# Kernel optimization log

Hardware: AMD Instinct MI355X
Metric: run time of the kernel (lower is better)

Reference implementation:

```python
import jax, jax.numpy as jnp
import numpy as np

H = 50  # hidden_size
IN = 1  # input_size

def _lstm_layer(x_tbi, w_ih, w_hh, b):
    # x_tbi: [T, B, in]; w_ih: [4H, in]; w_hh: [4H, H]; b: [4H] (b_ih + b_hh combined)
    T, B, _ = x_tbi.shape
    def step(carry, x_t):
        h, c = carry
        z = x_t @ w_ih.T + h @ w_hh.T + b  # [B, 4H]
        i, f, g, o = jnp.split(z, 4, axis=-1)
        i = jax.nn.sigmoid(i); f = jax.nn.sigmoid(f)
        g = jnp.tanh(g); o = jax.nn.sigmoid(o)
        c = f * c + i * g
        h = o * jnp.tanh(c)
        return (h, c), h
    h0 = jnp.zeros((B, H), x_tbi.dtype)
    c0 = jnp.zeros((B, H), x_tbi.dtype)
    _, hs = jax.lax.scan(step, (h0, c0), x_tbi)
    return hs  # [T, B, H]

def setup_inputs() -> dict:
    key = jax.random.key(0)
    ks = jax.random.split(key, 12)
    def u(k, shape, fan):
        s = 1.0 / np.sqrt(fan)
        return jax.random.uniform(k, shape, jnp.float32, -s, s)
    B, T = 2048, 512
    x = jax.random.normal(ks[0], (B, T, IN), jnp.float32)
    return {
        'x': x,
        'w_ih1': u(ks[1], (4 * H, IN), H), 'w_hh1': u(ks[2], (4 * H, H), H), 'b1': u(ks[3], (4 * H,), H),
        'w_ih2': u(ks[4], (4 * H, H), H), 'w_hh2': u(ks[5], (4 * H, H), H), 'b2': u(ks[6], (4 * H,), H),
        'w_ih3': u(ks[7], (4 * H, H), H), 'w_hh3': u(ks[8], (4 * H, H), H), 'b3': u(ks[9], (4 * H,), H),
        'w_fc': u(ks[10], (1, H), H), 'b_fc': u(ks[11], (1,), H),
    }

def reference(x, w_ih1, w_hh1, b1, w_ih2, w_hh2, b2, w_ih3, w_hh3, b3, w_fc, b_fc):
    # dropout layers act as identity in eval mode
    out = jnp.transpose(x, (1, 0, 2))  # [T, B, in]
    out = _lstm_layer(out, w_ih1, w_hh1, b1)
    out = _lstm_layer(out, w_ih2, w_hh2, b2)
    out = _lstm_layer(out, w_ih3, w_hh3, b3)
    last = out[-1]  # [B, H]
    return last @ w_fc.T + b_fc  # [B, 1]
```

## Files before the change

kernel.cpp:

```cpp
#include <hip/hip_runtime.h>
#include <math.h>

namespace {

constexpr int Hn = 50;
constexpr int Bn = 2048;
constexpr int Tn = 512;
constexpr int SW = 72;

constexpr float KS1f = -1.44269504088896340736f;
constexpr float KS2f = -2.88539008177792681472f;

typedef short short8 __attribute__((ext_vector_type(8)));
typedef float f32x4 __attribute__((ext_vector_type(4)));

__device__ __forceinline__ unsigned bcu(float f) { return __builtin_bit_cast(unsigned, f); }
__device__ __forceinline__ float bcf(unsigned u) { return __builtin_bit_cast(float, u); }
__device__ __forceinline__ float rcpa(float x) { return __builtin_amdgcn_rcpf(x); }

__device__ __forceinline__ float fexp2(float x) {
#if defined(__has_builtin)
#if __has_builtin(__builtin_amdgcn_exp2f)
  return __builtin_amdgcn_exp2f(x);
#else
  return exp2f(x);
#endif
#else
  return exp2f(x);
#endif
}

__device__ __forceinline__ void wsplit(short* ph, short* pl, float v) {
  const unsigned u = bcu(v);
  *ph = (short)(u >> 16);
  *pl = (short)(bcu(v - bcf(u & 0xFFFF0000u)) >> 16);
}

#define MF(a, b, c) __builtin_amdgcn_mfma_f32_16x16x32_bf16(a, b, c, 0, 0, 0)


#define LW(FI)                                                               \
  short8 FH##FI = {0, 0, 0, 0, 0, 0, 0, 0};                                  \
  short8 FL##FI = {0, 0, 0, 0, 0, 0, 0, 0};                                  \
  {                                                                          \
    const int tile_ =                                                        \
        ((FI) >= 16) ? ((L == 0 || wl != 0) ? 13 : 12)                       \
        : ((FI) >= 8) ? ((L == 0) ? 13 : (wl + 8))                           \
        : (L == 0)    ? (wl + 4 * ((FI) >> 1))                               \
                      : (wl + 4 * ((FI) >> 2));                              \
    const int chunk_ = ((FI) >= 8) ? ((FI)&3)                                \
                       : (L == 0)  ? ((FI)&1)                                \
                                   : ((FI)&3);                               \
    const int cb_ = 4 * tile_ + (nl >> 2);                                   \
    if (tile_ < 13 && cb_ < Hn) {                                            \
      const int row_ = (nl & 3) * Hn + cb_;                                  \
      const float sc_ = ((nl & 3) == 2) ? KS2f : KS1f;                       \
      _Pragma("unroll") for (int jj = 0; jj < 8; ++jj) {                     \
        const int k_ = 32 * chunk_ + quad * 8 + jj;                          \
        float wv = 0.f;                                                      \
        if (L == 0) {                                                        \
          if (k_ == 0) wv = wihL[row_];                                      \
          else if (k_ <= Hn) wv = whhL[row_ * Hn + k_ - 1];                  \
        } else if (L == 1) {                                                 \
          if (k_ >= 1 && k_ <= Hn) wv = wihL[row_ * Hn + k_ - 1];            \
          else if (k_ >= 64 && k_ < 64 + Hn) wv = whhL[row_ * Hn + k_ - 64]; \
        } else {                                                             \
          if (k_ < Hn) wv = wihL[row_ * Hn + k_];                            \
          else if (k_ >= 64 && k_ < 64 + Hn) wv = whhL[row_ * Hn + k_ - 64]; \
        }                                                                    \
        wv *= sc_;                                                           \
        const unsigned uu = bcu(wv);                                         \
        FH##FI[jj] = (short)(uu >> 16);                                      \
        FL##FI[jj] = (short)(bcu(wv - bcf(uu & 0xFFFF0000u)) >> 16);         \
      }                                                                      \
    }                                                                        \
  }

#define BINIT(J)                                                             \
  const int tile##J = wl + 4 * (J);                                          \
  const int tv##J = tile##J < 13;                                            \
  const int cell##J = 4 * tile##J + quad;                                    \
  float cs##J = 0.f, hl##J = 0.f;

#define STB(J)                                                               \
  if (tv##J) {                                                               \
    float b0_ = 0.f, b1_ = 0.f, b2_ = 0.f, b3_ = 0.f;                        \
    if (cell##J < Hn) {                                                      \
      b0_ = biasL[cell##J] * KS1f;                                           \
      b1_ = biasL[Hn + cell##J] * KS1f;                                      \
      b2_ = biasL[2 * Hn + cell##J] * KS2f;                                  \
      b3_ = biasL[3 * Hn + cell##J] * KS1f;                                  \
    }                                                                        \
    s_bv[w][J][quad][0] = b0_;                                               \
    s_bv[w][J][quad][1] = b1_;                                               \
    s_bv[w][J][quad][2] = b2_;                                               \
    s_bv[w][J][quad][3] = b3_;                                               \
  }

#define MTM(J, FI)                                                           \
  if (tv##J) {                                                               \
    ac##J = MF(FH##FI, uh_, ac##J);                                          \
    ac##J = MF(FL##FI, uh_, ac##J);                                          \
    ac##J = MF(FH##FI, ul_, ac##J);                                          \
  }

#define MTMS2(CI)                                                            \
  {                                                                          \
    const short8 fh_ = s_f4j2[wz2][wl][CI][0][lane];                         \
    const short8 fl_ = s_f4j2[wz2][wl][CI][1][lane];                         \
    ac2 = MF(fh_, uh_, ac2);                                                 \
    ac2 = MF(fl_, uh_, ac2);                                                 \
    ac2 = MF(fh_, ul_, ac2);                                                 \
  }

#define MTMS3(CI)                                                            \
  if (tv3) {                                                                 \
    const short8 fh_ = s_f4j3[wz2][CI][0][lane];                             \
    const short8 fl_ = s_f4j3[wz2][CI][1][lane];                             \
    ac3 = MF(fh_, uh_, ac3);                                                 \
    ac3 = MF(fl_, uh_, ac3);                                                 \
    ac3 = MF(fh_, ul_, ac3);                                                 \
  }

#define MCH_L1(LC, F0, F1, F2, F3)                                           \
  {                                                                          \
    const short8 uh_ = *(const short8*)&p1h[rb][nl][32 * (LC) + quad * 8];   \
    const short8 ul_ = *(const short8*)&p1l[rb][nl][32 * (LC) + quad * 8];   \
    MTM(0, F0) MTM(1, F1) MTM(2, F2) MTM(3, F3)                              \
  }

#define MCH_L23(PH, PL, LC, CI, F0, F1)                                      \
  {                                                                          \
    const short8 uh_ = *(const short8*)&PH[rb][nl][32 * (LC) + quad * 8];    \
    const short8 ul_ = *(const short8*)&PL[rb][nl][32 * (LC) + quad * 8];    \
    MTM(0, F0) MTM(1, F1) MTMS2(CI) MTMS3(CI)                                \
  }

#define CUP(J, PH, PL, KO)                                                   \
  if (tv##J) {                                                               \
    const float I_ = rcpa(1.0f + fexp2(ac##J[0]));                           \
    const float F_ = rcpa(1.0f + fexp2(ac##J[1]));                           \
    const float G_ = fmaf(2.0f, rcpa(1.0f + fexp2(ac##J[2])), -1.0f);        \
    const float O_ = rcpa(1.0f + fexp2(ac##J[3]));                           \
    cs##J = fmaf(F_, cs##J, I_ * G_);                                        \
    const float tc_ = fmaf(2.0f, rcpa(1.0f + fexp2(cs##J * KS2f)), -1.0f);   \
    const float hv = O_ * tc_;                                               \
    hl##J = hv;                                                              \
    if (cell##J < Hn)                                                        \
      wsplit(&PH[wb][nl][(KO) + cell##J], &PL[wb][nl][(KO) + cell##J], hv);  \
  }

__global__ __launch_bounds__(768, 3) void lstm_fused(
    const float* __restrict__ xg,
    const float* __restrict__ wih1, const float* __restrict__ whh1,
    const float* __restrict__ b1, const float* __restrict__ wih2,
    const float* __restrict__ whh2, const float* __restrict__ b2,
    const float* __restrict__ wih3, const float* __restrict__ whh3,
    const float* __restrict__ b3, const float* __restrict__ wfc,
    const float* __restrict__ bfc, float* __restrict__ out)
{
  __shared__ __align__(16) short p1h[2][16][SW];
  __shared__ __align__(16) short p1l[2][16][SW];
  __shared__ __align__(16) short p2h[2][16][SW];
  __shared__ __align__(16) short p2l[2][16][SW];
  __shared__ __align__(16) short p3h[2][16][SW];
  __shared__ __align__(16) short p3l[2][16][SW];
  __shared__ __align__(16) float s_bv[12][4][4][4];
  __shared__ __align__(16) short8 s_f4j2[2][4][4][2][64];
  __shared__ __align__(16) short8 s_f4j3[2][4][2][64];
  __shared__ float s_fc[4][16];

  const int tid = threadIdx.x;
  const int w = tid >> 6;
  const int lane = tid & 63;
  const int quad = lane >> 4;
  const int nl = lane & 15;
  const int L = (w < 4) ? 0 : (w < 8) ? 1 : 2;
  const int wl = w & 3;
  const int wz2 = (L == 2) ? 1 : 0;
  const int eb = blockIdx.x * 16;

  const float* wihL = (L == 0) ? wih1 : (L == 1) ? wih2 : wih3;
  const float* whhL = (L == 0) ? whh1 : (L == 1) ? whh2 : whh3;
  const float* biasL = (L == 0) ? b1 : (L == 1) ? b2 : b3;

  LW(0) LW(1) LW(2) LW(3) LW(4) LW(5) LW(6) LW(7)
  LW(8) LW(9) LW(10) LW(11)
  LW(16) LW(17) LW(18) LW(19)

  if (L > 0) {
    s_f4j2[wz2][wl][0][0][lane] = FH8;  s_f4j2[wz2][wl][0][1][lane] = FL8;
    s_f4j2[wz2][wl][1][0][lane] = FH9;  s_f4j2[wz2][wl][1][1][lane] = FL9;
    s_f4j2[wz2][wl][2][0][lane] = FH10; s_f4j2[wz2][wl][2][1][lane] = FL10;
    s_f4j2[wz2][wl][3][0][lane] = FH11; s_f4j2[wz2][wl][3][1][lane] = FL11;
    if (wl == 0) {
      s_f4j3[wz2][0][0][lane] = FH16; s_f4j3[wz2][0][1][lane] = FL16;
      s_f4j3[wz2][1][0][lane] = FH17; s_f4j3[wz2][1][1][lane] = FL17;
      s_f4j3[wz2][2][0][lane] = FH18; s_f4j3[wz2][2][1][lane] = FL18;
      s_f4j3[wz2][3][0][lane] = FH19; s_f4j3[wz2][3][1][lane] = FL19;
    }
  }

  BINIT(0) BINIT(1) BINIT(2) BINIT(3)

  for (int i = tid; i < 2 * 16 * SW; i += 768) {
    (&p1h[0][0][0])[i] = 0;
    (&p1l[0][0][0])[i] = 0;
    (&p2h[0][0][0])[i] = 0;
    (&p2l[0][0][0])[i] = 0;
    (&p3h[0][0][0])[i] = 0;
    (&p3l[0][0][0])[i] = 0;
  }
  for (int i = tid; i < 12 * 4 * 4 * 4; i += 768) (&s_bv[0][0][0][0])[i] = 0.f;
  __syncthreads();
  if (w == 0 && lane < 16) {
    const float xv = xg[(size_t)(eb + lane) * Tn + 0];
    wsplit(&p1h[0][lane][0], &p1l[0][lane][0], xv);
  }
  if (nl == 0) {
    STB(0) STB(1) STB(2) STB(3)
  }
  __syncthreads();

#pragma unroll 1
  for (int i = 0; i < Tn + 2; ++i) {
    const int rb = i & 1, wb = rb ^ 1;
    if (L == 0) {
      if (i < Tn) {
        float xv = 0.f;
        if (w == 0 && lane < 16 && i + 1 < Tn)
          xv = xg[(size_t)(eb + lane) * Tn + (i + 1)];
        f32x4 ac0 = *(const f32x4*)s_bv[w][0][quad];
        f32x4 ac1 = *(const f32x4*)s_bv[w][1][quad];
        f32x4 ac2 = *(const f32x4*)s_bv[w][2][quad];
        f32x4 ac3 = *(const f32x4*)s_bv[w][3][quad];
        __builtin_amdgcn_s_setprio(1);
        MCH_L1(0, 0, 2, 4, 6)
        MCH_L1(1, 1, 3, 5, 7)
        __builtin_amdgcn_s_setprio(0);
        CUP(0, p1h, p1l, 1)
        CUP(1, p1h, p1l, 1)
        CUP(2, p1h, p1l, 1)
        CUP(3, p1h, p1l, 1)
        if (w == 0 && lane < 16)
          wsplit(&p1h[wb][lane][0], &p1l[wb][lane][0], xv);
      }
    } else if (L == 1) {
      if (i >= 1 && i <= Tn) {
        f32x4 ac0 = *(const f32x4*)s_bv[w][0][quad];
        f32x4 ac1 = *(const f32x4*)s_bv[w][1][quad];
        f32x4 ac2 = *(const f32x4*)s_bv[w][2][quad];
        f32x4 ac3 = *(const f32x4*)s_bv[w][3][quad];
        __builtin_amdgcn_s_setprio(1);
        MCH_L23(p1h, p1l, 0, 0, 0, 4)
        MCH_L23(p1h, p1l, 1, 1, 1, 5)
        MCH_L23(p2h, p2l, 0, 2, 2, 6)
        MCH_L23(p2h, p2l, 1, 3, 3, 7)
        __builtin_amdgcn_s_setprio(0);
        CUP(0, p2h, p2l, 0)
        CUP(1, p2h, p2l, 0)
        CUP(2, p2h, p2l, 0)
        CUP(3, p2h, p2l, 0)
      }
    } else {
      if (i >= 2) {
        f32x4 ac0 = *(const f32x4*)s_bv[w][0][quad];
        f32x4 ac1 = *(const f32x4*)s_bv[w][1][quad];
        f32x4 ac2 = *(const f32x4*)s_bv[w][2][quad];
        f32x4 ac3 = *(const f32x4*)s_bv[w][3][quad];
        __builtin_amdgcn_s_setprio(1);
        MCH_L23(p2h, p2l, 0, 0, 0, 4)
        MCH_L23(p2h, p2l, 1, 1, 1, 5)
        MCH_L23(p3h, p3l, 0, 2, 2, 6)
        MCH_L23(p3h, p3l, 1, 3, 3, 7)
        __builtin_amdgcn_s_setprio(0);
        CUP(0, p3h, p3l, 0)
        CUP(1, p3h, p3l, 0)
        CUP(2, p3h, p3l, 0)
        CUP(3, p3h, p3l, 0)
      }
    }
    __syncthreads();
  }

  if (L == 2) {
    float pfc = 0.f;
    if (tv0 && cell0 < Hn) pfc += hl0 * wfc[cell0];
    if (tv1 && cell1 < Hn) pfc += hl1 * wfc[cell1];
    if (tv2 && cell2 < Hn) pfc += hl2 * wfc[cell2];
    if (tv3 && cell3 < Hn) pfc += hl3 * wfc[cell3];
    pfc += __shfl_xor(pfc, 16);
    pfc += __shfl_xor(pfc, 32);
    if (lane < 16) s_fc[wl][lane] = pfc;
  }
  __syncthreads();
  if (tid < 16)
    out[eb + tid] = bfc[0] + s_fc[0][tid] + s_fc[1][tid] + s_fc[2][tid] +
                    s_fc[3][tid];
}

}

extern "C" void kernel_launch(void* const* d_in, const int* in_sizes, int n_in,
                              void* d_out, int out_size, void* d_ws, size_t ws_size,
                              hipStream_t stream) {
  const float* x    = (const float*)d_in[0];
  const float* wih1 = (const float*)d_in[1];
  const float* whh1 = (const float*)d_in[2];
  const float* b1   = (const float*)d_in[3];
  const float* wih2 = (const float*)d_in[4];
  const float* whh2 = (const float*)d_in[5];
  const float* b2   = (const float*)d_in[6];
  const float* wih3 = (const float*)d_in[7];
  const float* whh3 = (const float*)d_in[8];
  const float* b3   = (const float*)d_in[9];
  const float* wfc  = (const float*)d_in[10];
  const float* bfc  = (const float*)d_in[11];
  float* out = (float*)d_out;

  lstm_fused<<<dim3(Bn / 16), dim3(768), 0, stream>>>(
      x, wih1, whh1, b1, wih2, whh2, b2, wih3, whh3, b3, wfc, bfc, out);
}
```

Baseline: 933.5 us.

## Fold bias into MFMA via constant-one input column; keep J2 fragments in AGPRs

Folds the per-gate bias into the weight fragments by adding a padding K column whose input is fixed at 1.0 (bf16 0x3F80). The MFMA accumulation then produces the bias term, and the per-step LDS loads of bias vectors are replaced by zero-initialised accumulators. The tile-2 weight fragments move from shared memory into registers, pinned to AGPRs with empty inline asm, which removes the per-step LDS reads for them. This raises register pressure and relies on padding columns 50 and 51 staying untouched by the hidden-state writes.

```diff
diff --git a/kernel.cpp b/kernel.cpp
--- a/kernel.cpp
+++ b/kernel.cpp
@@ -61,11 +61,14 @@
         if (L == 0) {                                                        \
           if (k_ == 0) wv = wihL[row_];                                      \
           else if (k_ <= Hn) wv = whhL[row_ * Hn + k_ - 1];                  \
+          else if (k_ == 51) wv = biasL[row_];                               \
         } else if (L == 1) {                                                 \
           if (k_ >= 1 && k_ <= Hn) wv = wihL[row_ * Hn + k_ - 1];            \
+          else if (k_ == 51) wv = biasL[row_];                               \
           else if (k_ >= 64 && k_ < 64 + Hn) wv = whhL[row_ * Hn + k_ - 64]; \
         } else {                                                             \
           if (k_ < Hn) wv = wihL[row_ * Hn + k_];                            \
+          else if (k_ == Hn) wv = biasL[row_];                               \
           else if (k_ >= 64 && k_ < 64 + Hn) wv = whhL[row_ * Hn + k_ - 64]; \
         }                                                                    \
         wv *= sc_;                                                           \
@@ -82,21 +85,6 @@
   const int cell##J = 4 * tile##J + quad;                                    \
   float cs##J = 0.f, hl##J = 0.f;
 
-#define STB(J)                                                               \
-  if (tv##J) {                                                               \
-    float b0_ = 0.f, b1_ = 0.f, b2_ = 0.f, b3_ = 0.f;                        \
-    if (cell##J < Hn) {                                                      \
-      b0_ = biasL[cell##J] * KS1f;                                           \
-      b1_ = biasL[Hn + cell##J] * KS1f;                                      \
-      b2_ = biasL[2 * Hn + cell##J] * KS2f;                                  \
-      b3_ = biasL[3 * Hn + cell##J] * KS1f;                                  \
-    }                                                                        \
-    s_bv[w][J][quad][0] = b0_;                                               \
-    s_bv[w][J][quad][1] = b1_;                                               \
-    s_bv[w][J][quad][2] = b2_;                                               \
-    s_bv[w][J][quad][3] = b3_;                                               \
-  }
-
 #define MTM(J, FI)                                                           \
   if (tv##J) {                                                               \
     ac##J = MF(FH##FI, uh_, ac##J);                                          \
@@ -106,11 +94,9 @@
 
 #define MTMS2(CI)                                                            \
   {                                                                          \
-    const short8 fh_ = s_f4j2[wz2][wl][CI][0][lane];                         \
-    const short8 fl_ = s_f4j2[wz2][wl][CI][1][lane];                         \
-    ac2 = MF(fh_, uh_, ac2);                                                 \
-    ac2 = MF(fl_, uh_, ac2);                                                 \
-    ac2 = MF(fh_, ul_, ac2);                                                 \
+    ac2 = MF(AJ2H##CI, uh_, ac2);                                            \
+    ac2 = MF(AJ2L##CI, uh_, ac2);                                            \
+    ac2 = MF(AJ2H##CI, ul_, ac2);                                            \
   }
 
 #define MTMS3(CI)                                                            \
@@ -165,8 +151,6 @@
   __shared__ __align__(16) short p2l[2][16][SW];
   __shared__ __align__(16) short p3h[2][16][SW];
   __shared__ __align__(16) short p3l[2][16][SW];
-  __shared__ __align__(16) float s_bv[12][4][4][4];
-  __shared__ __align__(16) short8 s_f4j2[2][4][4][2][64];
   __shared__ __align__(16) short8 s_f4j3[2][4][2][64];
   __shared__ float s_fc[4][16];
 
@@ -188,17 +172,18 @@
   LW(8) LW(9) LW(10) LW(11)
   LW(16) LW(17) LW(18) LW(19)
 
-  if (L > 0) {
-    s_f4j2[wz2][wl][0][0][lane] = FH8;  s_f4j2[wz2][wl][0][1][lane] = FL8;
-    s_f4j2[wz2][wl][1][0][lane] = FH9;  s_f4j2[wz2][wl][1][1][lane] = FL9;
-    s_f4j2[wz2][wl][2][0][lane] = FH10; s_f4j2[wz2][wl][2][1][lane] = FL10;
-    s_f4j2[wz2][wl][3][0][lane] = FH11; s_f4j2[wz2][wl][3][1][lane] = FL11;
-    if (wl == 0) {
-      s_f4j3[wz2][0][0][lane] = FH16; s_f4j3[wz2][0][1][lane] = FL16;
-      s_f4j3[wz2][1][0][lane] = FH17; s_f4j3[wz2][1][1][lane] = FL17;
-      s_f4j3[wz2][2][0][lane] = FH18; s_f4j3[wz2][2][1][lane] = FL18;
-      s_f4j3[wz2][3][0][lane] = FH19; s_f4j3[wz2][3][1][lane] = FL19;
-    }
+  short8 AJ2H0 = FH8,  AJ2L0 = FL8;
+  short8 AJ2H1 = FH9,  AJ2L1 = FL9;
+  short8 AJ2H2 = FH10, AJ2L2 = FL10;
+  short8 AJ2H3 = FH11, AJ2L3 = FL11;
+  asm volatile("" : "+a"(AJ2H0), "+a"(AJ2L0), "+a"(AJ2H1), "+a"(AJ2L1));
+  asm volatile("" : "+a"(AJ2H2), "+a"(AJ2L2), "+a"(AJ2H3), "+a"(AJ2L3));
+
+  if (L > 0 && wl == 0) {
+    s_f4j3[wz2][0][0][lane] = FH16; s_f4j3[wz2][0][1][lane] = FL16;
+    s_f4j3[wz2][1][0][lane] = FH17; s_f4j3[wz2][1][1][lane] = FL17;
+    s_f4j3[wz2][2][0][lane] = FH18; s_f4j3[wz2][2][1][lane] = FL18;
+    s_f4j3[wz2][3][0][lane] = FH19; s_f4j3[wz2][3][1][lane] = FL19;
   }
 
   BINIT(0) BINIT(1) BINIT(2) BINIT(3)
@@ -211,14 +196,15 @@
     (&p3h[0][0][0])[i] = 0;
     (&p3l[0][0][0])[i] = 0;
   }
-  for (int i = tid; i < 12 * 4 * 4 * 4; i += 768) (&s_bv[0][0][0][0])[i] = 0.f;
   __syncthreads();
   if (w == 0 && lane < 16) {
     const float xv = xg[(size_t)(eb + lane) * Tn + 0];
     wsplit(&p1h[0][lane][0], &p1l[0][lane][0], xv);
   }
-  if (nl == 0) {
-    STB(0) STB(1) STB(2) STB(3)
+  if (tid < 32) {
+    const int bb = tid >> 4, bn = tid & 15;
+    p1h[bb][bn][51] = (short)0x3F80;
+    p2h[bb][bn][50] = (short)0x3F80;
   }
   __syncthreads();
 
@@ -230,10 +216,10 @@
         float xv = 0.f;
         if (w == 0 && lane < 16 && i + 1 < Tn)
           xv = xg[(size_t)(eb + lane) * Tn + (i + 1)];
-        f32x4 ac0 = *(const f32x4*)s_bv[w][0][quad];
-        f32x4 ac1 = *(const f32x4*)s_bv[w][1][quad];
-        f32x4 ac2 = *(const f32x4*)s_bv[w][2][quad];
-        f32x4 ac3 = *(const f32x4*)s_bv[w][3][quad];
+        f32x4 ac0 = {0.f, 0.f, 0.f, 0.f};
+        f32x4 ac1 = {0.f, 0.f, 0.f, 0.f};
+        f32x4 ac2 = {0.f, 0.f, 0.f, 0.f};
+        f32x4 ac3 = {0.f, 0.f, 0.f, 0.f};
         __builtin_amdgcn_s_setprio(1);
         MCH_L1(0, 0, 2, 4, 6)
         MCH_L1(1, 1, 3, 5, 7)
@@ -247,10 +233,10 @@
       }
     } else if (L == 1) {
       if (i >= 1 && i <= Tn) {
-        f32x4 ac0 = *(const f32x4*)s_bv[w][0][quad];
-        f32x4 ac1 = *(const f32x4*)s_bv[w][1][quad];
-        f32x4 ac2 = *(const f32x4*)s_bv[w][2][quad];
-        f32x4 ac3 = *(const f32x4*)s_bv[w][3][quad];
+        f32x4 ac0 = {0.f, 0.f, 0.f, 0.f};
+        f32x4 ac1 = {0.f, 0.f, 0.f, 0.f};
+        f32x4 ac2 = {0.f, 0.f, 0.f, 0.f};
+        f32x4 ac3 = {0.f, 0.f, 0.f, 0.f};
         __builtin_amdgcn_s_setprio(1);
         MCH_L23(p1h, p1l, 0, 0, 0, 4)
         MCH_L23(p1h, p1l, 1, 1, 1, 5)
@@ -264,10 +250,10 @@
       }
     } else {
       if (i >= 2) {
-        f32x4 ac0 = *(const f32x4*)s_bv[w][0][quad];
-        f32x4 ac1 = *(const f32x4*)s_bv[w][1][quad];
-        f32x4 ac2 = *(const f32x4*)s_bv[w][2][quad];
-        f32x4 ac3 = *(const f32x4*)s_bv[w][3][quad];
+        f32x4 ac0 = {0.f, 0.f, 0.f, 0.f};
+        f32x4 ac1 = {0.f, 0.f, 0.f, 0.f};
+        f32x4 ac2 = {0.f, 0.f, 0.f, 0.f};
+        f32x4 ac3 = {0.f, 0.f, 0.f, 0.f};
         __builtin_amdgcn_s_setprio(1);
         MCH_L23(p2h, p2l, 0, 0, 0, 4)
         MCH_L23(p2h, p2l, 1, 1, 1, 5)
```

Measured after the change: 949.6 us. Within noise of the previous version (+1.7%).
